# Optimization experiments

Hardware: AMD Instinct MI355X
Metric: run time of the kernel (lower is better)

## Reference

```python
import jax, jax.numpy as jnp
import numpy as np
import itertools
from itertools import combinations

N_QUBITS = 6
DIM = 2 ** N_QUBITS            # 64
N_GEN = DIM ** 2 - 1           # 4095 (SU(2^n) generators)
K_LOCAL = 2
OBS_DIM = 2 ** K_LOCAL         # 4
WIRE_GROUPS = [list(c) for c in combinations(range(N_QUBITS), K_LOCAL)]
N_OBS = len(WIRE_GROUPS)       # 15
N_OFF = OBS_DIM * (OBS_DIM - 1) // 2  # 6
CHUNK_DIM = 512
T_EMB = 256
HID = 256
BATCH = 512

# lower-triangle (i>j) flat ordering used by create_Hermitian: c = i*(i-1)/2 + j
_TRI_R = np.array([i for i in range(1, OBS_DIM) for j in range(i)])
_TRI_C = np.array([j for i in range(1, OBS_DIM) for j in range(i)])
_DIAG = np.arange(OBS_DIM - 1)  # diag slots 0..N-2 get 2*D[1..N-1]; last diag is 0


def _pauli_basis():
    """Lexicographic Pauli words on N_QUBITS qubits, identity excluded -> (N_GEN, DIM, DIM)."""
    I = np.eye(2, dtype=np.complex64)
    X = np.array([[0, 1], [1, 0]], dtype=np.complex64)
    Y = np.array([[0, -1j], [1j, 0]], dtype=np.complex64)
    Z = np.array([[1, 0], [0, -1]], dtype=np.complex64)
    P1 = {'I': I, 'X': X, 'Y': Y, 'Z': Z}
    out = np.empty((N_GEN, DIM, DIM), dtype=np.complex64)
    k = 0
    for word in itertools.product('IXYZ', repeat=N_QUBITS):
        if all(c == 'I' for c in word):
            continue
        m = np.array([[1.0 + 0j]], dtype=np.complex64)
        for c in word:
            m = np.kron(m, P1[c])
        out[k] = m
        k += 1
    return jnp.asarray(out)


def setup_inputs() -> dict:
    key = jax.random.key(0)
    ks = jax.random.split(key, 12)
    inp = {
        'x': jax.random.normal(ks[0], (BATCH, CHUNK_DIM + T_EMB), dtype=jnp.float32),
        # enc_proj: Linear(768,256) -> SiLU -> Linear(256,4095)
        'W1': jax.random.normal(ks[1], (CHUNK_DIM + T_EMB, HID), dtype=jnp.float32) * 0.02,
        'b1': jnp.zeros((HID,), dtype=jnp.float32),
        'W2': jax.random.normal(ks[2], (HID, N_GEN), dtype=jnp.float32) * 0.02,
        'b2': jnp.zeros((N_GEN,), dtype=jnp.float32),
        # ANO Hermitian params (std=2.0 per torch init)
        'Aoff': jax.random.normal(ks[3], (N_OBS, N_OFF), dtype=jnp.float32) * 2.0,
        'Boff': jax.random.normal(ks[4], (N_OBS, N_OFF), dtype=jnp.float32) * 2.0,
        'Ddiag': jax.random.normal(ks[5], (N_OBS, OBS_DIM), dtype=jnp.float32) * 2.0,
        # vel_head: Linear(15,256) -> SiLU -> Linear(256,512)
        'Wv1': jax.random.normal(ks[6], (N_OBS, HID), dtype=jnp.float32) * 0.02,
        'bv1': jnp.zeros((HID,), dtype=jnp.float32),
        'Wv2': jax.random.normal(ks[7], (HID, CHUNK_DIM), dtype=jnp.float32) * 0.02,
        'bv2': jnp.zeros((CHUNK_DIM,), dtype=jnp.float32),
        'pauli': _pauli_basis(),  # fixed SU(2^n) generator basis (constant)
    }
    return inp


def _build_H(Aoff, Boff, Ddiag):
    """Batched create_Hermitian: (N_OBS, 4, 4) complex. h + h^H semantics."""
    H = jnp.zeros((N_OBS, OBS_DIM, OBS_DIM), dtype=jnp.complex64)
    off = Aoff.astype(jnp.complex64) + 1j * Boff.astype(jnp.complex64)
    H = H.at[:, _TRI_R, _TRI_C].set(off)
    H = H + jnp.conj(jnp.swapaxes(H, -1, -2))
    H = H.at[:, _DIAG, _DIAG].set((2.0 * Ddiag[:, 1:]).astype(jnp.complex64))
    return H


def _forward(x, W1, b1, W2, b2, Aoff, Boff, Ddiag, Wv1, bv1, Wv2, bv2, pauli):
    B = x.shape[0]
    # enc_proj MLP -> SU(2^n) angles theta (B, 4095)
    enc = jax.nn.silu(x @ W1 + b1) @ W2 + b2
    # SpecialUnitary: U = exp(i * sum_m theta_m P_m); apply to |0...0> via eigh of the
    # Hermitian effective generator H_eff = sum_m theta_m P_m.
    H_eff = jnp.einsum('bm,mij->bij', enc.astype(jnp.complex64), pauli)  # (B, 64, 64)
    lam, V = jnp.linalg.eigh(H_eff)
    # psi = V @ diag(exp(i*lam)) @ V^dag @ e0 ; (V^dag e0)_j = conj(V[0, j])
    psi = jnp.einsum('bij,bj->bi', V, jnp.exp(1j * lam.astype(jnp.complex64)) * jnp.conj(V[:, 0, :]))
    H = _build_H(Aoff, Boff, Ddiag)  # (15, 4, 4)
    psi_t = psi.reshape((B,) + (2,) * N_QUBITS)
    q = []
    for w, (a, b) in enumerate(WIRE_GROUPS):
        # bring wires (a,b) to front (wire order: first wire is most significant bit)
        pg = jnp.moveaxis(psi_t, (1 + a, 1 + b), (1, 2)).reshape(B, OBS_DIM, -1)
        # <H> = tr(rho H), rho_kl = sum_r psi[k,r] conj(psi[l,r])
        q.append(jnp.einsum('bkr,blr,lk->b', pg, jnp.conj(pg), H[w]).real)
    q = jnp.stack(q, axis=1).astype(jnp.float32)  # (B, 15)
    return jax.nn.silu(q @ Wv1 + bv1) @ Wv2 + bv2  # (B, 512)


def reference(x, W1, b1, W2, b2, Aoff, Boff, Ddiag, Wv1, bv1, Wv2, bv2, pauli):
    return _forward(x, W1, b1, W2, b2, Aoff, Boff, Ddiag, Wv1, bv1, Wv2, bv2, pauli)
```

## Files before the change

### kernel.cpp

```cpp
#include <hip/hip_runtime.h>
#include <hip/hip_bf16.h>

#define BATCH   512
#define INDIM   768
#define HID     256
#define NGEN    4095
#define NGENP   4096
#define NOBS    15
#define OUTDIM  512
#define DIM     64

typedef __hip_bfloat16 bf16;

__device__ int      g_isf32;
__device__ float    g_theta[(size_t)BATCH*NGENP];
__device__ float    g_q[BATCH*NOBS];
__device__ float    g_h[(size_t)BATCH*HID];
__device__ float    g_xp[(size_t)BATCH*INDIM];
__device__ float    g_W1p[(size_t)INDIM*HID];
__device__ float    g_b1p[HID];
__device__ float    g_W2p[(size_t)HID*NGENP];
__device__ float    g_b2p[NGENP];

__device__ __forceinline__ float tof(bf16 v){ return __bfloat162float(v); }
__device__ __forceinline__ float silu(float x){ return x / (1.f + __expf(-x)); }
__device__ __forceinline__ float blo(unsigned u){ return __uint_as_float(u<<16); }
__device__ __forceinline__ float bhi(unsigned u){ return __uint_as_float(u & 0xFFFF0000u); }

template<bool F32>
__device__ __forceinline__ float LD(const void* p, size_t i){
  if(F32) return ((const float*)p)[i];
  else    return tof(((const bf16*)p)[i]);
}

__device__ __forceinline__ unsigned spread6(unsigned x){
  return (x&1u) | ((x&2u)<<1) | ((x&4u)<<2) | ((x&8u)<<3) | ((x&16u)<<4) | ((x&32u)<<5);
}

__constant__ int c_WA[15] = {0,0,0,0,0,1,1,1,1,2,2,2,3,3,4};
__constant__ int c_WB[15] = {1,2,3,4,5,2,3,4,5,3,4,5,4,5,5};
__constant__ int c_Lt[6]  = {1,2,2,3,3,3};
__constant__ int c_Kt[6]  = {0,0,1,0,1,2};

__global__ __launch_bounds__(256) void k_detect(const unsigned* __restrict__ w1raw){
  __shared__ int sh[256];
  const int t = threadIdx.x;
  int c = 0;
  for(int i=t;i<1024;i+=256){
    unsigned ub = (w1raw[i]>>8) & 0x7Fu;
    if(ub>=0x30u && ub<=0x3Fu) c++;
  }
  sh[t] = c;
  __syncthreads();
  for(int s=128;s>0;s>>=1){
    if(t<s) sh[t] += sh[t+s];
    __syncthreads();
  }
  if(t==0) g_isf32 = (sh[0] < 512) ? 1 : 0;
}

template<bool F32>
__device__ void pack_body(const void* __restrict__ x, const void* __restrict__ W1,
                          const void* __restrict__ b1, const void* __restrict__ W2,
                          const void* __restrict__ b2){
  const size_t gid = (size_t)blockIdx.x*256 + threadIdx.x;
  const size_t stride = (size_t)gridDim.x*256;
  for(size_t i=gid;i<(size_t)BATCH*INDIM;i+=stride) g_xp[i]  = LD<F32>(x,i);
  for(size_t i=gid;i<(size_t)INDIM*HID;i+=stride)   g_W1p[i] = LD<F32>(W1,i);
  for(size_t i=gid;i<HID;i+=stride)                 g_b1p[i] = LD<F32>(b1,i);
  for(size_t i=gid;i<(size_t)HID*NGENP;i+=stride){
    size_t k = i>>12, c = i&4095;
    g_W2p[i] = (c<NGEN) ? LD<F32>(W2,k*NGEN+c) : 0.f;
  }
  for(size_t i=gid;i<NGENP;i+=stride) g_b2p[i] = (i<NGEN) ? LD<F32>(b2,i) : 0.f;
}

__global__ __launch_bounds__(256) void k_pack(const void* x,const void* W1,const void* b1,
                                              const void* W2,const void* b2){
  if(g_isf32) pack_body<true >(x,W1,b1,W2,b2);
  else        pack_body<false>(x,W1,b1,W2,b2);
}

__global__ __launch_bounds__(256) void k_enc1(){
  __shared__ __align__(16) float xl[INDIM][4];
  const int t = threadIdx.x, b0 = blockIdx.x*4;
  for(int i=t;i<4*INDIM;i+=256){
    int r = i/INDIM, k = i - r*INDIM;
    xl[k][r] = g_xp[(size_t)(b0+r)*INDIM + k];
  }
  __syncthreads();
  const int rh = t>>7, tc = t&127;
  float a00=0.f,a01=0.f,a10=0.f,a11=0.f;
  for(int k0=0;k0<INDIM;k0+=8){
    #pragma unroll
    for(int u=0;u<8;u++){
      float2 wv = *(const float2*)&g_W1p[(size_t)(k0+u)*HID + 2*tc];
      float2 xv = *(const float2*)&xl[k0+u][2*rh];
      a00 += xv.x*wv.x; a01 += xv.x*wv.y;
      a10 += xv.y*wv.x; a11 += xv.y*wv.y;
    }
  }
  const float bb0 = g_b1p[2*tc], bb1 = g_b1p[2*tc+1];
  g_h[(size_t)(b0+2*rh+0)*HID + 2*tc+0] = silu(a00+bb0);
  g_h[(size_t)(b0+2*rh+0)*HID + 2*tc+1] = silu(a01+bb1);
  g_h[(size_t)(b0+2*rh+1)*HID + 2*tc+0] = silu(a10+bb0);
  g_h[(size_t)(b0+2*rh+1)*HID + 2*tc+1] = silu(a11+bb1);
}

__global__ __launch_bounds__(512) void k_enc2(){
  __shared__ __align__(16) float hl[HID][8];
  const int t  = threadIdx.x;
  const int b0 = (blockIdx.x>>2)*8;
  const int c0 = (blockIdx.x&3)*1024;
  for(int i=t;i<8*HID;i+=512){
    int r = i>>8, k = i&255;
    hl[k][r] = g_h[(size_t)(b0+r)*HID + k];
  }
  __syncthreads();
  const int rh = t>>8, tc = t&255;
  const int col = c0 + 4*tc;
  float4 bv = *(const float4*)&g_b2p[col];
  float acc[4][4];
  #pragma unroll
  for(int i=0;i<4;i++){ acc[i][0]=bv.x; acc[i][1]=bv.y; acc[i][2]=bv.z; acc[i][3]=bv.w; }
  for(int k0=0;k0<HID;k0+=8){
    #pragma unroll
    for(int u=0;u<8;u++){
      float4 wv = *(const float4*)&g_W2p[(size_t)(k0+u)*NGENP + col];
      float4 hv = *(const float4*)&hl[k0+u][4*rh];
      acc[0][0]+=hv.x*wv.x; acc[0][1]+=hv.x*wv.y; acc[0][2]+=hv.x*wv.z; acc[0][3]+=hv.x*wv.w;
      acc[1][0]+=hv.y*wv.x; acc[1][1]+=hv.y*wv.y; acc[1][2]+=hv.y*wv.z; acc[1][3]+=hv.y*wv.w;
      acc[2][0]+=hv.z*wv.x; acc[2][1]+=hv.z*wv.y; acc[2][2]+=hv.z*wv.z; acc[2][3]+=hv.z*wv.w;
      acc[3][0]+=hv.w*wv.x; acc[3][1]+=hv.w*wv.y; acc[3][2]+=hv.w*wv.z; acc[3][3]+=hv.w*wv.w;
    }
  }
  #pragma unroll
  for(int i=0;i<4;i++){
    float4 o = make_float4(acc[i][0],acc[i][1],acc[i][2],acc[i][3]);
    *(float4*)&g_theta[(size_t)(b0+4*rh+i)*NGENP + col] = o;
  }
}

template<bool F32>
__device__ void state_body(const void* __restrict__ Aoff, const void* __restrict__ Boff,
                           const void* __restrict__ Ddiag,
                           const void* __restrict__ Wv1, const void* __restrict__ bv1,
                           const void* __restrict__ Wv2, const void* __restrict__ bv2,
                           void* __restrict__ out, char* sm){
  float*  th   = (float*)sm;
  float*  HH   = (float*)(sm + 16384);
  typedef float2 rep_t[66];
  rep_t*  vrA  = (rep_t*)sm;
  rep_t*  vrB  = (rep_t*)(sm + 2112);
  float2* ps   = (float2*)(sm + 4224);
  float2* coef = (float2*)(sm + 4736);
  float*  rs   = (float*)(sm + 6016);
  float*  qacc = (float*)(sm + 6272);
  float*  s_inva = (float*)(sm + 6336);
  int*    s_K    = (int*)(sm + 6340);
  float*  s_aG   = (float*)(sm + 6344);
  float*  hl   = (float*)(sm + 6400);
  float (*part)[64][8] = (float(*)[64][8])(sm + 7424);
  float*  n11  = (float*)(sm + 15616);
  float*  n12  = (float*)(sm + 15872);

  const int b = blockIdx.x, t = threadIdx.x;
  for(int m=t;m<NGEN;m+=256) th[m] = g_theta[(size_t)b*NGENP+m];
  __syncthreads();

  const int lane = t & 63, wav = t >> 6;
  for(int it=0; it<16; ++it){
    int d = (it<<2) | wav;
    unsigned td = (unsigned)(lane & d);
    unsigned tn = (unsigned)(lane & ~d) & 63u;
    unsigned w  = spread6((unsigned)d) + spread6(td) + 3u*spread6(tn);
    float thv = (w==0u) ? 0.f : th[w-1u];
    int ny = __popc(td) & 3;
    float gr = (ny==0)?  thv : (ny==2 ? -thv : 0.f);
    float gi = (ny==1)? -thv : (ny==3 ?  thv : 0.f);
    #pragma unroll
    for(int s=1;s<64;s<<=1){
      float pr = __shfl_xor(gr, s);
      float pi = __shfl_xor(gi, s);
      if(lane & s){ gr = pr - gr; gi = pi - gi; }
      else        { gr = gr + pr; gi = gi + pi; }
    }
    int j = lane ^ d;
    HH[lane*132 + 2*j]   = gr;
    HH[lane*132 + 2*j+1] = gi;
  }
  __syncthreads();

  const int i = t >> 2, c = t & 3, j0 = c*16;
  float hreg[32];
  float rsum = 0.f;
  #pragma unroll
  for(int jj=0;jj<16;jj+=2){
    float4 hv = *(const float4*)&HH[i*132 + 2*(j0+jj)];
    hreg[2*jj+0]=hv.x; hreg[2*jj+1]=hv.y; hreg[2*jj+2]=hv.z; hreg[2*jj+3]=hv.w;
    rsum += fabsf(hv.x)+fabsf(hv.y)+fabsf(hv.z)+fabsf(hv.w);
  }
  rsum += __shfl_xor(rsum,1);
  rsum += __shfl_xor(rsum,2);
  if(c==0) rs[i] = rsum;
  __syncthreads();

  if(t==0){
    float aG = 0.5f;
    for(int r=0;r<DIM;r++) aG = fmaxf(aG, rs[r]);
    *s_aG = aG;
  }
  __syncthreads();
  const float aG    = *s_aG;
  const float invaG = 1.f/aG;

  {
    rep_t* pv1 = vrA;
    rep_t* pv0 = vrB;
    if(t < DIM){
      float2 e0v = make_float2(t==0?1.f:0.f, 0.f);
      #pragma unroll
      for(int cc=0;cc<4;cc++) pv1[cc][t] = e0v;
    }
    __syncthreads();
    for(int m=1;m<=12;++m){
      const float* vb = (const float*)&pv1[c][0];
      float yr=0.f, yi=0.f;
      #pragma unroll
      for(int jj=0;jj<16;jj+=2){
        float4 xv = *(const float4*)&vb[2*(j0+jj)];
        float hr0=hreg[2*jj], hi0=hreg[2*jj+1], hr1=hreg[2*jj+2], hi1=hreg[2*jj+3];
        yr += hr0*xv.x - hi0*xv.y;
        yi += hr0*xv.y + hi0*xv.x;
        yr += hr1*xv.z - hi1*xv.w;
        yi += hr1*xv.w + hi1*xv.z;
      }
      yr += __shfl_xor(yr,1); yr += __shfl_xor(yr,2);
      yi += __shfl_xor(yi,1); yi += __shfl_xor(yi,2);
      if(c==0){
        float vnr = invaG*yr, vni = invaG*yi;
        float2 vn = make_float2(vnr, vni);
        #pragma unroll
        for(int cc=0;cc<4;cc++) pv0[cc][i] = vn;
        if(m==11) n11[i] = vnr*vnr + vni*vni;
        if(m==12) n12[i] = vnr*vnr + vni*vni;
      }
      __syncthreads();
      rep_t* tmp = pv0; pv0 = pv1; pv1 = tmp;
    }
  }

  if(t==0){
    float s11=0.f, s12=0.f;
    for(int r=0;r<DIM;r++){ s11 += n11[r]; s12 += n12[r]; }
    float a = aG;
    if(s11 > 1e-30f){
      float ratio = sqrtf(s12/s11);
      float ap = 1.35f * ratio * aG;
      a = fminf(aG, fmaxf(ap, 0.5f));
    }
    int K = (int)ceilf(a + 6.f*cbrtf(a) + 10.f);
    if(K>150) K=150;
    float bkp=0.f, bk=1e-35f, snorm=0.f;
    for(int k=K+12;k>=1;--k){
      float bkm = (2.f*(float)k/a)*bk - bkp;
      int n = k-1;
      if(n<=K) coef[n].x = bkm;
      if((n&1)==0) snorm += (n==0?1.f:2.f)*bkm;
      bkp = bk; bk = bkm;
    }
    float invs = 1.f/snorm;
    for(int n=0;n<=K;n++){
      float cv = coef[n].x*invs*(n==0?1.f:2.f);
      int p = n&3;
      float cr = (p==0)? cv : (p==2 ? -cv : 0.f);
      float ci = (p==1)? cv : (p==3 ? -cv : 0.f);
      coef[n] = make_float2(cr,ci);
    }
    *s_K = K;
    *s_inva = 1.f/a;
  }
  __syncthreads();
  const float inva = *s_inva;
  const int K = *s_K;

  rep_t* v0r = vrA;
  rep_t* v1r = vrB;
  if(t < DIM){
    float2 w1 = make_float2(HH[t*132+0]*inva, HH[t*132+1]*inva);
    float2 e0 = make_float2(t==0?1.f:0.f, 0.f);
    #pragma unroll
    for(int cc=0;cc<4;cc++){ v0r[cc][t] = e0; v1r[cc][t] = w1; }
    float2 c0 = coef[0], c1 = coef[1];
    float2 p;
    p.x = (t==0?c0.x:0.f) + c1.x*w1.x - c1.y*w1.y;
    p.y = (t==0?c0.y:0.f) + c1.x*w1.y + c1.y*w1.x;
    ps[t] = p;
  }
  __syncthreads();

  for(int k=2;k<=K;k++){
    const float* vb = (const float*)&v1r[c][0];
    float yr=0.f, yi=0.f;
    #pragma unroll
    for(int jj=0;jj<16;jj+=2){
      float4 xv = *(const float4*)&vb[2*(j0+jj)];
      float hr0=hreg[2*jj], hi0=hreg[2*jj+1], hr1=hreg[2*jj+2], hi1=hreg[2*jj+3];
      yr += hr0*xv.x - hi0*xv.y;
      yi += hr0*xv.y + hi0*xv.x;
      yr += hr1*xv.z - hi1*xv.w;
      yi += hr1*xv.w + hi1*xv.z;
    }
    yr += __shfl_xor(yr,1); yr += __shfl_xor(yr,2);
    yi += __shfl_xor(yi,1); yi += __shfl_xor(yi,2);
    if(c==0){
      float2 vm = v0r[0][i];
      float2 vn = make_float2(2.f*inva*yr - vm.x, 2.f*inva*yi - vm.y);
      #pragma unroll
      for(int cc=0;cc<4;cc++) v0r[cc][i] = vn;
      float2 ck = coef[k];
      float2 p = ps[i];
      p.x += ck.x*vn.x - ck.y*vn.y;
      p.y += ck.x*vn.y + ck.y*vn.x;
      ps[i] = p;
    }
    __syncthreads();
    rep_t* tmp = v0r; v0r = v1r; v1r = tmp;
  }

  if(t<NOBS) qacc[t]=0.f;
  __syncthreads();

  if(t<150){
    int w = t/10, s = t%10;
    int posA = 5 - c_WA[w], posB = 5 - c_WB[w];
    float contrib = 0.f;
    bool have = false;
    if(s<4){
      int kk = s;
      if(kk<3){
        float val = 0.f;
        for(int r=0;r<16;r++){
          int idx = (((kk>>1)&1)<<posA) | ((kk&1)<<posB);
          int rb = 3;
          #pragma unroll
          for(int p=5;p>=0;--p){
            if(p==posA || p==posB) continue;
            idx |= ((r>>rb)&1)<<p;
            rb--;
          }
          float2 pv = ps[idx];
          val += pv.x*pv.x + pv.y*pv.y;
        }
        contrib = val*2.f*LD<F32>(Ddiag, w*4 + kk + 1);
        have = true;
      }
    } else {
      int cc = s-4;
      int l = c_Lt[cc], kk = c_Kt[cc];
      float zr=0.f, zi=0.f;
      for(int r=0;r<16;r++){
        int idxk = (((kk>>1)&1)<<posA) | ((kk&1)<<posB);
        int idxl = (((l >>1)&1)<<posA) | ((l &1)<<posB);
        int rb = 3;
        #pragma unroll
        for(int p=5;p>=0;--p){
          if(p==posA || p==posB) continue;
          int bit = (r>>rb)&1;
          idxk |= bit<<p; idxl |= bit<<p;
          rb--;
        }
        float2 pk = ps[idxk], pl = ps[idxl];
        zr += pk.x*pl.x + pk.y*pl.y;
        zi += pk.y*pl.x - pk.x*pl.y;
      }
      contrib = 2.f*(zr*LD<F32>(Aoff,w*6+cc) - zi*LD<F32>(Boff,w*6+cc));
      have = true;
    }
    if(have) atomicAdd(&qacc[w], contrib);
  }
  __syncthreads();
  if(t<NOBS) g_q[(size_t)b*NOBS + t] = qacc[t];

  if(!F32){
    {
      float acc = tof(((const bf16*)bv1)[t]);
      #pragma unroll
      for(int k=0;k<NOBS;k++) acc += qacc[k]*tof(((const bf16*)Wv1)[k*HID+t]);
      hl[t] = silu(acc);
    }
    __syncthreads();
    const int rg = t >> 6;
    const uint4* w2v = (const uint4*)Wv2;
    float a8[8] = {0.f,0.f,0.f,0.f,0.f,0.f,0.f,0.f};
    for(int kk=0; kk<64; kk+=8){
      uint4 wv[8];
      #pragma unroll
      for(int u=0;u<8;u++) wv[u] = w2v[(size_t)(rg*64+kk+u)*64 + lane];
      #pragma unroll
      for(int u=0;u<8;u++){
        float hk = hl[rg*64+kk+u];
        a8[0] += hk*blo(wv[u].x); a8[1] += hk*bhi(wv[u].x);
        a8[2] += hk*blo(wv[u].y); a8[3] += hk*bhi(wv[u].y);
        a8[4] += hk*blo(wv[u].z); a8[5] += hk*bhi(wv[u].z);
        a8[6] += hk*blo(wv[u].w); a8[7] += hk*bhi(wv[u].w);
      }
    }
    #pragma unroll
    for(int j=0;j<8;j++) part[rg][lane][j] = a8[j];
    __syncthreads();
    {
      int cA = 2*t, cB = 2*t+1;
      float vA = tof(((const bf16*)bv2)[cA]);
      float vB = tof(((const bf16*)bv2)[cB]);
      #pragma unroll
      for(int r2=0;r2<4;r2++){
        vA += part[r2][cA>>3][cA&7];
        vB += part[r2][cB>>3][cB&7];
      }
      bf16 ha = __float2bfloat16(vA), hb = __float2bfloat16(vB);
      unsigned pw = (unsigned)(*(unsigned short*)&ha) |
                    ((unsigned)(*(unsigned short*)&hb)<<16);
      ((unsigned*)out)[(size_t)b*(OUTDIM/2) + t] = pw;
    }
  }
}

__global__ __launch_bounds__(256) void k_state(const void* Aoff,const void* Boff,const void* Dd,
                                               const void* Wv1,const void* bv1,
                                               const void* Wv2,const void* bv2, void* out){
  __shared__ __align__(16) char sm[50176];
  if(g_isf32) state_body<true >(Aoff,Boff,Dd,Wv1,bv1,Wv2,bv2,out,sm);
  else        state_body<false>(Aoff,Boff,Dd,Wv1,bv1,Wv2,bv2,out,sm);
}

template<bool F32>
__device__ void vel_body(const void* __restrict__ Wv1, const void* __restrict__ bv1,
                         const void* __restrict__ Wv2, const void* __restrict__ bv2,
                         void* __restrict__ out){
  const int b = blockIdx.x, t = threadIdx.x;
  if(F32){
    __shared__ float ql[NOBS];
    __shared__ float hl[HID];
    if(t<NOBS) ql[t] = g_q[(size_t)b*NOBS+t];
    __syncthreads();
    float acc = LD<F32>(bv1,t);
    #pragma unroll
    for(int k=0;k<NOBS;k++) acc += ql[k]*LD<F32>(Wv1,k*HID+t);
    hl[t] = silu(acc);
    __syncthreads();
    #pragma unroll
    for(int oo=0;oo<2;oo++){
      int o = t + oo*256;
      float s0=0.f;
      for(int k=0;k<HID;k++) s0 += hl[k]*LD<F32>(Wv2,(size_t)k*OUTDIM+o);
      ((float*)out)[(size_t)b*OUTDIM+o] = LD<F32>(bv2,o) + s0;
    }
  }
}

__global__ __launch_bounds__(256) void k_vel(const void* Wv1,const void* bv1,
                                             const void* Wv2,const void* bv2, void* out){
  if(g_isf32) vel_body<true >(Wv1,bv1,Wv2,bv2,out);
  else        vel_body<false>(Wv1,bv1,Wv2,bv2,out);
}

extern "C" void kernel_launch(void* const* d_in, const int* in_sizes, int n_in,
                              void* d_out, int out_size, void* d_ws, size_t ws_size,
                              hipStream_t stream){
  const void* x    = d_in[0];
  const void* W1   = d_in[1];
  const void* b1   = d_in[2];
  const void* W2   = d_in[3];
  const void* b2   = d_in[4];
  const void* Aoff = d_in[5];
  const void* Boff = d_in[6];
  const void* Dd   = d_in[7];
  const void* Wv1  = d_in[8];
  const void* bv1  = d_in[9];
  const void* Wv2  = d_in[10];
  const void* bv2  = d_in[11];

  k_detect<<<1,256,0,stream>>>((const unsigned*)W1);
  k_pack <<<1024,256,0,stream>>>(x,W1,b1,W2,b2);
  k_enc1 <<<BATCH/4,256,0,stream>>>();
  k_enc2 <<<256,512,0,stream>>>();
  k_state<<<BATCH,256,0,stream>>>(Aoff,Boff,Dd,Wv1,bv1,Wv2,bv2,d_out);
  k_vel  <<<BATCH,256,0,stream>>>(Wv1,bv1,Wv2,bv2,d_out);
}
```

Before: 266.9 us.

## Fuse dtype detection, packing, enc1 and velocity MLP to cut kernel launches

Drops the separate detect kernel; each block now runs its own in-kernel dtype detection with a wave-shuffle reduction. The first encoder layer is fused into the packing kernel, reading x and W1 directly without staging copies, and the f32 velocity MLP is fused into the state kernel so g_q and k_vel go away. This saves three launches and several global round-trips. In exchange every block re-reads 4 KB of W1 for detection, and the packing blocks now also carry enc1 work.

```diff
diff --git a/kernel.cpp b/kernel.cpp
--- a/kernel.cpp
+++ b/kernel.cpp
@@ -12,13 +12,8 @@
 
 typedef __hip_bfloat16 bf16;
 
-__device__ int      g_isf32;
 __device__ float    g_theta[(size_t)BATCH*NGENP];
-__device__ float    g_q[BATCH*NOBS];
 __device__ float    g_h[(size_t)BATCH*HID];
-__device__ float    g_xp[(size_t)BATCH*INDIM];
-__device__ float    g_W1p[(size_t)INDIM*HID];
-__device__ float    g_b1p[HID];
 __device__ float    g_W2p[(size_t)HID*NGENP];
 __device__ float    g_b2p[NGENP];
 
@@ -33,6 +28,24 @@
   else    return tof(((const bf16*)p)[i]);
 }
 
+__device__ __forceinline__ bool detect_f32(const unsigned* __restrict__ w1raw, int* red){
+  const int t = threadIdx.x & (blockDim.x-1);
+  const int lane = t & 63, wav = t >> 6;
+  int c = 0;
+  for(int i=t;i<1024;i+=(int)blockDim.x){
+    unsigned ub = (w1raw[i]>>8) & 0x7Fu;
+    if(ub>=0x30u && ub<=0x3Fu) c++;
+  }
+  #pragma unroll
+  for(int s=1;s<64;s<<=1) c += __shfl_xor(c, s);
+  if(lane==0) red[wav] = c;
+  __syncthreads();
+  int nw = (int)blockDim.x >> 6;
+  int tot = 0;
+  for(int w=0;w<nw;w++) tot += red[w];
+  return tot < 512;
+}
+
 __device__ __forceinline__ unsigned spread6(unsigned x){
   return (x&1u) | ((x&2u)<<1) | ((x&4u)<<2) | ((x&8u)<<3) | ((x&16u)<<4) | ((x&32u)<<5);
 }
@@ -42,69 +55,60 @@
 __constant__ int c_Lt[6]  = {1,2,2,3,3,3};
 __constant__ int c_Kt[6]  = {0,0,1,0,1,2};
 
-__global__ __launch_bounds__(256) void k_detect(const unsigned* __restrict__ w1raw){
-  __shared__ int sh[256];
+template<bool F32>
+__device__ void prep_body(const void* __restrict__ x, const void* __restrict__ W1,
+                          const void* __restrict__ b1, const void* __restrict__ W2,
+                          const void* __restrict__ b2, float (*xl)[4]){
   const int t = threadIdx.x;
-  int c = 0;
-  for(int i=t;i<1024;i+=256){
-    unsigned ub = (w1raw[i]>>8) & 0x7Fu;
-    if(ub>=0x30u && ub<=0x3Fu) c++;
-  }
-  sh[t] = c;
-  __syncthreads();
-  for(int s=128;s>0;s>>=1){
-    if(t<s) sh[t] += sh[t+s];
-    __syncthreads();
-  }
-  if(t==0) g_isf32 = (sh[0] < 512) ? 1 : 0;
-}
-
-template<bool F32>
-__device__ void pack_body(const void* __restrict__ x, const void* __restrict__ W1,
-                          const void* __restrict__ b1, const void* __restrict__ W2,
-                          const void* __restrict__ b2){
-  const size_t gid = (size_t)blockIdx.x*256 + threadIdx.x;
+  const size_t gid = (size_t)blockIdx.x*256 + t;
   const size_t stride = (size_t)gridDim.x*256;
-  for(size_t i=gid;i<(size_t)BATCH*INDIM;i+=stride) g_xp[i]  = LD<F32>(x,i);
-  for(size_t i=gid;i<(size_t)INDIM*HID;i+=stride)   g_W1p[i] = LD<F32>(W1,i);
-  for(size_t i=gid;i<HID;i+=stride)                 g_b1p[i] = LD<F32>(b1,i);
+
   for(size_t i=gid;i<(size_t)HID*NGENP;i+=stride){
     size_t k = i>>12, c = i&4095;
     g_W2p[i] = (c<NGEN) ? LD<F32>(W2,k*NGEN+c) : 0.f;
   }
   for(size_t i=gid;i<NGENP;i+=stride) g_b2p[i] = (i<NGEN) ? LD<F32>(b2,i) : 0.f;
-}
-
-__global__ __launch_bounds__(256) void k_pack(const void* x,const void* W1,const void* b1,
+
+  if(blockIdx.x < BATCH/4){
+    const int b0 = blockIdx.x*4;
+    for(int i=t;i<4*INDIM;i+=256){
+      int r = i/INDIM, k = i - r*INDIM;
+      xl[k][r] = LD<F32>(x,(size_t)(b0+r)*INDIM + k);
+    }
+    __syncthreads();
+    const int rh = t>>7, tc = t&127;
+    float a00=0.f,a01=0.f,a10=0.f,a11=0.f;
+    for(int k0=0;k0<INDIM;k0+=8){
+      #pragma unroll
+      for(int u=0;u<8;u++){
+        float wvx, wvy;
+        if(F32){
+          float2 wv = *(const float2*)&((const float*)W1)[(size_t)(k0+u)*HID + 2*tc];
+          wvx = wv.x; wvy = wv.y;
+        } else {
+          unsigned w = ((const unsigned*)W1)[(size_t)(k0+u)*(HID/2) + tc];
+          wvx = blo(w); wvy = bhi(w);
+        }
+        float2 xv = *(const float2*)&xl[k0+u][2*rh];
+        a00 += xv.x*wvx; a01 += xv.x*wvy;
+        a10 += xv.y*wvx; a11 += xv.y*wvy;
+      }
+    }
+    const float bb0 = LD<F32>(b1,2*tc), bb1 = LD<F32>(b1,2*tc+1);
+    g_h[(size_t)(b0+2*rh+0)*HID + 2*tc+0] = silu(a00+bb0);
+    g_h[(size_t)(b0+2*rh+0)*HID + 2*tc+1] = silu(a01+bb1);
+    g_h[(size_t)(b0+2*rh+1)*HID + 2*tc+0] = silu(a10+bb0);
+    g_h[(size_t)(b0+2*rh+1)*HID + 2*tc+1] = silu(a11+bb1);
+  }
+}
+
+__global__ __launch_bounds__(256) void k_prep(const void* x,const void* W1,const void* b1,
                                               const void* W2,const void* b2){
-  if(g_isf32) pack_body<true >(x,W1,b1,W2,b2);
-  else        pack_body<false>(x,W1,b1,W2,b2);
-}
-
-__global__ __launch_bounds__(256) void k_enc1(){
   __shared__ __align__(16) float xl[INDIM][4];
-  const int t = threadIdx.x, b0 = blockIdx.x*4;
-  for(int i=t;i<4*INDIM;i+=256){
-    int r = i/INDIM, k = i - r*INDIM;
-    xl[k][r] = g_xp[(size_t)(b0+r)*INDIM + k];
-  }
-  __syncthreads();
-  const int rh = t>>7, tc = t&127;
-  float a00=0.f,a01=0.f,a10=0.f,a11=0.f;
-  for(int k0=0;k0<INDIM;k0+=8){
-    #pragma unroll
-    for(int u=0;u<8;u++){
-      float2 wv = *(const float2*)&g_W1p[(size_t)(k0+u)*HID + 2*tc];
-      float2 xv = *(const float2*)&xl[k0+u][2*rh];
-      a00 += xv.x*wv.x; a01 += xv.x*wv.y;
-      a10 += xv.y*wv.x; a11 += xv.y*wv.y;
-    }
-  }
-  const float bb0 = g_b1p[2*tc], bb1 = g_b1p[2*tc+1];
-  g_h[(size_t)(b0+2*rh+0)*HID + 2*tc+0] = silu(a00+bb0);
-  g_h[(size_t)(b0+2*rh+0)*HID + 2*tc+1] = silu(a01+bb1);
-  g_h[(size_t)(b0+2*rh+1)*HID + 2*tc+0] = silu(a10+bb0);
-  g_h[(size_t)(b0+2*rh+1)*HID + 2*tc+1] = silu(a11+bb1);
+  __shared__ int red[4];
+  bool isf32 = detect_f32((const unsigned*)W1, red);
+  if(isf32) prep_body<true >(x,W1,b1,W2,b2,xl);
+  else      prep_body<false>(x,W1,b1,W2,b2,xl);
 }
 
 __global__ __launch_bounds__(512) void k_enc2(){
@@ -380,7 +384,6 @@
     if(have) atomicAdd(&qacc[w], contrib);
   }
   __syncthreads();
-  if(t<NOBS) g_q[(size_t)b*NOBS + t] = qacc[t];
 
   if(!F32){
     {
@@ -423,46 +426,33 @@
                     ((unsigned)(*(unsigned short*)&hb)<<16);
       ((unsigned*)out)[(size_t)b*(OUTDIM/2) + t] = pw;
     }
-  }
-}
-
-__global__ __launch_bounds__(256) void k_state(const void* Aoff,const void* Boff,const void* Dd,
+  } else {
+    {
+      float acc = ((const float*)bv1)[t];
+      #pragma unroll
+      for(int k=0;k<NOBS;k++) acc += qacc[k]*((const float*)Wv1)[k*HID+t];
+      hl[t] = silu(acc);
+    }
+    __syncthreads();
+    #pragma unroll
+    for(int oo=0;oo<2;oo++){
+      int o = t + oo*256;
+      float s0=0.f;
+      for(int k=0;k<HID;k++) s0 += hl[k]*((const float*)Wv2)[(size_t)k*OUTDIM+o];
+      ((float*)out)[(size_t)b*OUTDIM+o] = ((const float*)bv2)[o] + s0;
+    }
+  }
+}
+
+__global__ __launch_bounds__(256) void k_state(const void* W1raw,
+                                               const void* Aoff,const void* Boff,const void* Dd,
                                                const void* Wv1,const void* bv1,
                                                const void* Wv2,const void* bv2, void* out){
   __shared__ __align__(16) char sm[50176];
-  if(g_isf32) state_body<true >(Aoff,Boff,Dd,Wv1,bv1,Wv2,bv2,out,sm);
-  else        state_body<false>(Aoff,Boff,Dd,Wv1,bv1,Wv2,bv2,out,sm);
-}
-
-template<bool F32>
-__device__ void vel_body(const void* __restrict__ Wv1, const void* __restrict__ bv1,
-                         const void* __restrict__ Wv2, const void* __restrict__ bv2,
-                         void* __restrict__ out){
-  const int b = blockIdx.x, t = threadIdx.x;
-  if(F32){
-    __shared__ float ql[NOBS];
-    __shared__ float hl[HID];
-    if(t<NOBS) ql[t] = g_q[(size_t)b*NOBS+t];
-    __syncthreads();
-    float acc = LD<F32>(bv1,t);
-    #pragma unroll
-    for(int k=0;k<NOBS;k++) acc += ql[k]*LD<F32>(Wv1,k*HID+t);
-    hl[t] = silu(acc);
-    __syncthreads();
-    #pragma unroll
-    for(int oo=0;oo<2;oo++){
-      int o = t + oo*256;
-      float s0=0.f;
-      for(int k=0;k<HID;k++) s0 += hl[k]*LD<F32>(Wv2,(size_t)k*OUTDIM+o);
-      ((float*)out)[(size_t)b*OUTDIM+o] = LD<F32>(bv2,o) + s0;
-    }
-  }
-}
-
-__global__ __launch_bounds__(256) void k_vel(const void* Wv1,const void* bv1,
-                                             const void* Wv2,const void* bv2, void* out){
-  if(g_isf32) vel_body<true >(Wv1,bv1,Wv2,bv2,out);
-  else        vel_body<false>(Wv1,bv1,Wv2,bv2,out);
+  __shared__ int red[4];
+  bool isf32 = detect_f32((const unsigned*)W1raw, red);
+  if(isf32) state_body<true >(Aoff,Boff,Dd,Wv1,bv1,Wv2,bv2,out,sm);
+  else      state_body<false>(Aoff,Boff,Dd,Wv1,bv1,Wv2,bv2,out,sm);
 }
 
 extern "C" void kernel_launch(void* const* d_in, const int* in_sizes, int n_in,
@@ -481,10 +471,7 @@
   const void* Wv2  = d_in[10];
   const void* bv2  = d_in[11];
 
-  k_detect<<<1,256,0,stream>>>((const unsigned*)W1);
-  k_pack <<<1024,256,0,stream>>>(x,W1,b1,W2,b2);
-  k_enc1 <<<BATCH/4,256,0,stream>>>();
+  k_prep <<<1024,256,0,stream>>>(x,W1,b1,W2,b2);
   k_enc2 <<<256,512,0,stream>>>();
-  k_state<<<BATCH,256,0,stream>>>(Aoff,Boff,Dd,Wv1,bv1,Wv2,bv2,d_out);
-  k_vel  <<<BATCH,256,0,stream>>>(Wv1,bv1,Wv2,bv2,d_out);
-}
+  k_state<<<BATCH,256,0,stream>>>(W1,Aoff,Boff,Dd,Wv1,bv1,Wv2,bv2,d_out);
+}
```

Result: slower. 275.5 us (+3.2%).
